# Optimization experiments

Hardware: AMD Instinct MI355X
Metric: run time of the kernel (lower is better)

The kernel has to match this reference:

```python
import jax, jax.numpy as jnp
import numpy as np

# Kobayashi dendrite-growth parameters (init_params values from the repo)
TAU = 3e-4
EPSILONB = 0.01
KAPPA = 1.8
DELTA = 0.02
ANISO = 6.0
ALPHA = 0.9
GAMMA = 10.0
TEQ = 1.0
THETA0 = 0.2
PIX = 4.0 * np.arctan(1.0)  # pi
DX = 0.03
DY = 0.03
DT = 1e-4

B, H, W = 4, 2048, 2048


def lap(u, dx, dy):
    # 5-point Laplacian, periodic boundaries. x = last axis, y = second-to-last.
    return ((jnp.roll(u, -1, -1) + jnp.roll(u, 1, -1) - 2.0 * u) / (dx * dx)
            + (jnp.roll(u, -1, -2) + jnp.roll(u, 1, -2) - 2.0 * u) / (dy * dy))


def grad(u, axis_name, d):
    ax = -1 if axis_name == 'x' else -2
    return (jnp.roll(u, -1, ax) - jnp.roll(u, 1, ax)) / (2.0 * d)


def setup_inputs() -> dict:
    key = jax.random.key(0)
    k1, k2 = jax.random.split(key)
    phi = jax.random.uniform(k1, (B, H, W), dtype=jnp.float32)
    tempr = jax.random.uniform(k2, (B, H, W), dtype=jnp.float32)
    return {"phi": phi, "tempr": tempr}


def reference(phi, tempr):
    lap_phi = lap(phi, DX, DY)
    lap_tempr = lap(tempr, DX, DY)
    phidx = grad(phi, 'x', DX)
    phidy = grad(phi, 'y', DY)
    theta = jnp.arctan2(phidy, phidx)
    epsilon = EPSILONB * (1.0 + DELTA * jnp.cos(ANISO * (theta - THETA0)))
    epsilon_deriv = -EPSILONB * ANISO * DELTA * jnp.sin(ANISO * (theta - THETA0))
    prod_mat1 = epsilon * epsilon_deriv * phidx
    prod_mat2 = -epsilon * epsilon_deriv * phidy
    term1 = grad(prod_mat1, 'y', DY)
    term2 = grad(prod_mat2, 'x', DX)
    m = ALPHA / PIX * jnp.arctan(GAMMA * (TEQ - tempr))
    dphi_dt = DT / TAU * (term1 + term2 + epsilon ** 2 * lap_phi
                          + phi * (1.0 - phi) * (phi - 0.5 + m))
    phi_new = phi + dphi_dt
    tempr_new = tempr + DT * lap_tempr + KAPPA * dphi_dt
    return (phi_new, tempr_new)
```

## Files before the change

### kernel.cpp

```cpp
#include <hip/hip_runtime.h>
#include <hip/hip_fp16.h>
#include <math.h>


#define Bz 4
#define Hd 2048
#define Wd 2048
#define TX 64
#define TY 32
#define PW 68
#define PH 36
#define QW 66
#define QH 34

#define INVD2   1111.11111111111f
#define K1      277.777777777778f
#define DT_TAU  0.333333333333333f
#define DTc     1e-4f
#define KAPPAc  1.8f
#define EPSB    0.01f
#define DELTAc  0.02f
#define ANISOc  6.0f
#define A_PI    0.2864788975654116f
#define GAMMAc  10.0f
#define TEQc    1.0f
#define C6T0    0.3623577544766736f
#define S6T0    0.9320390859672263f
#define PI_2    1.5707963267948966f
#define SC      65536.0f
#define ISC     (1.0f/65536.0f)

__device__ __forceinline__ void prodc(float dx, float dy,
                                      float& p1s, float& p2s, float& e2s)
{
    float dx2 = dx * dx;
    float r2  = fmaf(dy, dy, dx2);
    float cn  = fmaf(-dy, dy, dx2);
    float irr = __builtin_amdgcn_rcpf(fmaxf(r2, 1e-20f));
    float c2  = cn * irr;
    float s2  = 2.0f * dx * dy * irr;
    float c22 = c2 * c2;
    float s22 = s2 * s2;
    float c6  = c2 * fmaf(4.0f, c22, -3.0f);
    float s6  = s2 * fmaf(-4.0f, s22, 3.0f);
    float cosA = fmaf(c6, C6T0, s6 * S6T0);
    float sinA = fmaf(s6, C6T0, -c6 * S6T0);
    float eps  = fmaf(EPSB * DELTAc, cosA, EPSB);
    float eesc = eps * (-EPSB * ANISOc * DELTAc * SC) * sinA;
    p1s = eesc * dx;
    p2s = -eesc * dy;
    e2s = eps * eps * SC;
}

__device__ __forceinline__ float atan_fast(float g) {
    float r  = __builtin_amdgcn_rcpf(g);
    float a  = fminf(g, r);
    float a2 = a * a;
    float p  = a * fmaf(a2, fmaf(a2, 0.079331f, -0.288679f), 0.995354f);
    return (g <= 1.0f) ? p : PI_2 - p;
}

__global__ __launch_bounds__(256, 8) void dendrite_step(
    const float* __restrict__ phi, const float* __restrict__ tempr,
    float* __restrict__ out_phi, float* __restrict__ out_tempr)
{
    __shared__ __half2 sphi2[PH * PW / 2];
    __shared__ __half2 spk[QH * QW];
    __shared__ __half2 se2_2[QH * QW / 2];

    const int tid = threadIdx.x;
    const int x0 = blockIdx.x * TX;
    const int y0 = blockIdx.y * TY;
    const int base = blockIdx.z * (Hd * Wd);

    for (int i = tid; i < PH * PW / 2; i += 256) {
        int r = i / (PW / 2);
        int c2 = i - r * (PW / 2);
        int gy = (y0 + r - 2) & (Hd - 1);
        int gx = (x0 + 2 * c2 - 2) & (Wd - 1);
        float2 v = *(const float2*)(phi + base + gy * Wd + gx);
        sphi2[i] = __floats2half2_rn(v.x, v.y);
    }
    __syncthreads();

    const __half* sph = (const __half*)sphi2;
    for (int i = tid; i < QH * (QW / 2); i += 256) {
        int r = i / (QW / 2);
        int c2 = i - r * (QW / 2);
        int cQ = 2 * c2;
        int rowc = (r + 1) * (PW / 2) + c2;
        __half2 A  = sphi2[rowc];
        __half2 Bv = sphi2[rowc + 1];
        __half2 U0 = sphi2[rowc - PW / 2];
        __half2 U1 = sphi2[rowc - PW / 2 + 1];
        __half2 D0 = sphi2[rowc + PW / 2];
        __half2 D1 = sphi2[rowc + PW / 2 + 1];

        float f0 = __low2float(A),  f1 = __high2float(A);
        float f2 = __low2float(Bv), f3 = __high2float(Bv);

        float p1a, p2a, e2a, p1b, p2b, e2b;
        prodc(f2 - f0, __high2float(D0) - __high2float(U0), p1a, p2a, e2a);
        prodc(f3 - f1, __low2float(D1)  - __low2float(U1),  p1b, p2b, e2b);

        int q = r * QW + cQ;
        spk[q]     = __floats2half2_rn(p1a, p2a);
        spk[q + 1] = __floats2half2_rn(p1b, p2b);
        se2_2[r * (QW / 2) + c2] = __floats2half2_rn(e2a, e2b);
    }
    __syncthreads();

    const __half* se2h = (const __half*)se2_2;
    const int tx = tid & 63;
    const int tg = tid >> 6;
    const int ys = tg * 8;
    const int col = tx + 2;
    const int gx = x0 + tx;
    const int gxm = (gx - 1) & (Wd - 1);
    const int gxp = (gx + 1) & (Wd - 1);

    float pm = __half2float(sph[(ys + 1) * PW + col]);
    float pc_ = __half2float(sph[(ys + 2) * PW + col]);
    float s1m = __low2float(spk[ys * QW + tx + 1]);
    float s1c = __low2float(spk[(ys + 1) * QW + tx + 1]);

    float tm = tempr[base + ((y0 + ys - 1) & (Hd - 1)) * Wd + gx];
    int rb0 = base + (y0 + ys) * Wd;
    float tcl = tempr[rb0 + gxm];
    float tcc = tempr[rb0 + gx];
    float tcr = tempr[rb0 + gxp];
    int rb1 = base + ((y0 + ys + 1) & (Hd - 1)) * Wd;
    float tnl = tempr[rb1 + gxm];
    float tnc = tempr[rb1 + gx];
    float tnr = tempr[rb1 + gxp];

    for (int k = 0; k < 8; ++k) {
        int y = ys + k;
        int qrow = y + 1;
        int prow = y + 2;

        float t2l = 0.0f, t2c = 0.0f, t2r = 0.0f;
        if (k < 7) {
            int rb2 = base + ((y0 + y + 2) & (Hd - 1)) * Wd;
            t2l = tempr[rb2 + gxm];
            t2c = tempr[rb2 + gx];
            t2r = tempr[rb2 + gxp];
        }

        float pp  = __half2float(sph[(prow + 1) * PW + col]);
        float pl  = __half2float(sph[prow * PW + col - 1]);
        float prr = __half2float(sph[prow * PW + col + 1]);
        float lap_phi = (pl + prr + pm + pp - 4.0f * pc_) * INVD2;

        float s1p  = __low2float(spk[(qrow + 1) * QW + tx + 1]);
        float sp2l = __high2float(spk[qrow * QW + tx]);
        float sp2r = __high2float(spk[qrow * QW + tx + 2]);
        float term12 = (s1p - s1m + sp2r - sp2l) * (K1 * ISC);
        float e2 = __half2float(se2h[qrow * QW + tx + 1]) * ISC;

        float lap_t = (tcl + tcr + tm + tnc - 4.0f * tcc) * INVD2;

        float mm = A_PI * atan_fast(GAMMAc * (TEQc - tcc));
        float dphi = DT_TAU * (term12 + e2 * lap_phi
                               + pc_ * (1.0f - pc_) * (pc_ - 0.5f + mm));

        int gidx = base + (y0 + y) * Wd + gx;
        out_phi[gidx] = pc_ + dphi;
        out_tempr[gidx] = fmaf(KAPPAc, dphi, fmaf(DTc, lap_t, tcc));

        pm = pc_; pc_ = pp;
        s1m = s1c; s1c = s1p;
        tm = tcc;
        tcl = tnl; tcc = tnc; tcr = tnr;
        tnl = t2l; tnc = t2c; tnr = t2r;
    }
}

extern "C" void kernel_launch(void* const* d_in, const int* in_sizes, int n_in,
                              void* d_out, int out_size, void* d_ws, size_t ws_size,
                              hipStream_t stream) {
    const float* phi = (const float*)d_in[0];
    const float* tempr = (const float*)d_in[1];
    float* out_phi = (float*)d_out;
    float* out_tempr = out_phi + (size_t)Bz * Hd * Wd;

    dim3 grid(Wd / TX, Hd / TY, Bz);
    dendrite_step<<<grid, 256, 0, stream>>>(phi, tempr, out_phi, out_tempr);
}
```

Measured before the change: 240.6 us.

## Process two columns per thread with vectorized half2/float2 LDS and global access

Each thread now computes two adjacent x-columns across 4 rows instead of one column across 8 rows. Shared-memory padding is widened to 4 columns so halo reads align to half2. Reads and writes of phi/products, tempr and outputs become 2-wide vector accesses, and neighbour values are shared between the pair. This targets LDS instruction count and global transaction count, at the cost of more registers per thread and shorter row-streaming reuse.

```diff
diff --git a/kernel.cpp b/kernel.cpp
--- a/kernel.cpp
+++ b/kernel.cpp
@@ -8,9 +8,10 @@
 #define Wd 2048
 #define TX 64
 #define TY 32
-#define PW 68
+#define PW 72
 #define PH 36
-#define QW 66
+#define PW2 (PW/2)
+#define QW 68
 #define QH 34
 
 #define INVD2   1111.11111111111f
@@ -60,119 +61,166 @@
     return (g <= 1.0f) ? p : PI_2 - p;
 }
 
+__device__ __forceinline__ void ldq2(const __half2* p,
+                                     float& f1a, float& f2a,
+                                     float& f1b, float& f2b)
+{
+    uint2 v = *reinterpret_cast<const uint2*>(p);
+    __half2 a = *reinterpret_cast<__half2*>(&v.x);
+    __half2 b = *reinterpret_cast<__half2*>(&v.y);
+    f1a = __low2float(a); f2a = __high2float(a);
+    f1b = __low2float(b); f2b = __high2float(b);
+}
+
 __global__ __launch_bounds__(256, 8) void dendrite_step(
     const float* __restrict__ phi, const float* __restrict__ tempr,
     float* __restrict__ out_phi, float* __restrict__ out_tempr)
 {
-    __shared__ __half2 sphi2[PH * PW / 2];
+    __shared__ __half2 sphi2[PH * PW2];
     __shared__ __half2 spk[QH * QW];
-    __shared__ __half2 se2_2[QH * QW / 2];
+    __shared__ __half  se2[QH * QW];
 
     const int tid = threadIdx.x;
     const int x0 = blockIdx.x * TX;
     const int y0 = blockIdx.y * TY;
     const int base = blockIdx.z * (Hd * Wd);
 
-    for (int i = tid; i < PH * PW / 2; i += 256) {
-        int r = i / (PW / 2);
-        int c2 = i - r * (PW / 2);
+    for (int i = tid; i < PH * PW2; i += 256) {
+        int r = i / PW2;
+        int c2 = i - r * PW2;
         int gy = (y0 + r - 2) & (Hd - 1);
-        int gx = (x0 + 2 * c2 - 2) & (Wd - 1);
+        int gx = (x0 + 2 * c2 - 4) & (Wd - 1);
         float2 v = *(const float2*)(phi + base + gy * Wd + gx);
         sphi2[i] = __floats2half2_rn(v.x, v.y);
     }
     __syncthreads();
 
-    const __half* sph = (const __half*)sphi2;
     for (int i = tid; i < QH * (QW / 2); i += 256) {
         int r = i / (QW / 2);
-        int c2 = i - r * (QW / 2);
-        int cQ = 2 * c2;
-        int rowc = (r + 1) * (PW / 2) + c2;
-        __half2 A  = sphi2[rowc];
-        __half2 Bv = sphi2[rowc + 1];
-        __half2 U0 = sphi2[rowc - PW / 2];
-        __half2 U1 = sphi2[rowc - PW / 2 + 1];
-        __half2 D0 = sphi2[rowc + PW / 2];
-        __half2 D1 = sphi2[rowc + PW / 2 + 1];
-
-        float f0 = __low2float(A),  f1 = __high2float(A);
-        float f2 = __low2float(Bv), f3 = __high2float(Bv);
+        int j = i - r * (QW / 2);
+        int rowc = (r + 1) * PW2 + j;
+        __half2 P0 = sphi2[rowc];
+        __half2 P1 = sphi2[rowc + 1];
+        __half2 P2 = sphi2[rowc + 2];
+        __half2 U  = sphi2[rowc - PW2 + 1];
+        __half2 D  = sphi2[rowc + PW2 + 1];
+
+        float dx0 = __high2float(P1) - __high2float(P0);
+        float dx1 = __low2float(P2)  - __low2float(P1);
+        float dy0 = __low2float(D)   - __low2float(U);
+        float dy1 = __high2float(D)  - __high2float(U);
 
         float p1a, p2a, e2a, p1b, p2b, e2b;
-        prodc(f2 - f0, __high2float(D0) - __high2float(U0), p1a, p2a, e2a);
-        prodc(f3 - f1, __low2float(D1)  - __low2float(U1),  p1b, p2b, e2b);
-
-        int q = r * QW + cQ;
+        prodc(dx0, dy0, p1a, p2a, e2a);
+        prodc(dx1, dy1, p1b, p2b, e2b);
+
+        int q = r * QW + 2 * j;
         spk[q]     = __floats2half2_rn(p1a, p2a);
         spk[q + 1] = __floats2half2_rn(p1b, p2b);
-        se2_2[r * (QW / 2) + c2] = __floats2half2_rn(e2a, e2b);
+        *reinterpret_cast<__half2*>(se2 + q) = __floats2half2_rn(e2a, e2b);
     }
     __syncthreads();
 
-    const __half* se2h = (const __half*)se2_2;
-    const int tx = tid & 63;
-    const int tg = tid >> 6;
-    const int ys = tg * 8;
-    const int col = tx + 2;
-    const int gx = x0 + tx;
-    const int gxm = (gx - 1) & (Wd - 1);
-    const int gxp = (gx + 1) & (Wd - 1);
-
-    float pm = __half2float(sph[(ys + 1) * PW + col]);
-    float pc_ = __half2float(sph[(ys + 2) * PW + col]);
-    float s1m = __low2float(spk[ys * QW + tx + 1]);
-    float s1c = __low2float(spk[(ys + 1) * QW + tx + 1]);
-
-    float tm = tempr[base + ((y0 + ys - 1) & (Hd - 1)) * Wd + gx];
+    const int tx2 = tid & 31;
+    const int tg  = tid >> 5;
+    const int ys  = tg * 4;
+    const int c0  = tx2 * 2;
+    const int qc0 = c0 + 2;
+    const int pctr = (c0 + 4) >> 1;
+    const int gx0 = x0 + c0;
+    const int gxm = (gx0 - 1) & (Wd - 1);
+    const int gxp = (gx0 + 2) & (Wd - 1);
+
+    float pm0, pm1, pc0, pc1;
+    {
+        __half2 a = sphi2[(ys + 1) * PW2 + pctr];
+        __half2 b = sphi2[(ys + 2) * PW2 + pctr];
+        pm0 = __low2float(a); pm1 = __high2float(a);
+        pc0 = __low2float(b); pc1 = __high2float(b);
+    }
+
+    float s1m0 = __low2float(spk[ys * QW + qc0]);
+    float s1m1 = __low2float(spk[ys * QW + qc0 + 1]);
+    float s1c0, p2c0, s1c1, p2c1;
+    ldq2(spk + (ys + 1) * QW + qc0, s1c0, p2c0, s1c1, p2c1);
+
+    float tm0, tm1;
+    {
+        float2 t = *(const float2*)(tempr + base + ((y0 + ys - 1) & (Hd - 1)) * Wd + gx0);
+        tm0 = t.x; tm1 = t.y;
+    }
     int rb0 = base + (y0 + ys) * Wd;
     float tcl = tempr[rb0 + gxm];
-    float tcc = tempr[rb0 + gx];
+    float2 tc0v = *(const float2*)(tempr + rb0 + gx0);
+    float tcc0 = tc0v.x, tcc1 = tc0v.y;
     float tcr = tempr[rb0 + gxp];
     int rb1 = base + ((y0 + ys + 1) & (Hd - 1)) * Wd;
     float tnl = tempr[rb1 + gxm];
-    float tnc = tempr[rb1 + gx];
+    float2 tn0v = *(const float2*)(tempr + rb1 + gx0);
+    float tnc0 = tn0v.x, tnc1 = tn0v.y;
     float tnr = tempr[rb1 + gxp];
 
-    for (int k = 0; k < 8; ++k) {
+    for (int k = 0; k < 4; ++k) {
         int y = ys + k;
         int qrow = y + 1;
         int prow = y + 2;
 
-        float t2l = 0.0f, t2c = 0.0f, t2r = 0.0f;
-        if (k < 7) {
+        float t2l = 0.0f, t2c0 = 0.0f, t2c1 = 0.0f, t2r = 0.0f;
+        if (k < 3) {
             int rb2 = base + ((y0 + y + 2) & (Hd - 1)) * Wd;
             t2l = tempr[rb2 + gxm];
-            t2c = tempr[rb2 + gx];
+            float2 t2 = *(const float2*)(tempr + rb2 + gx0);
+            t2c0 = t2.x; t2c1 = t2.y;
             t2r = tempr[rb2 + gxp];
         }
 
-        float pp  = __half2float(sph[(prow + 1) * PW + col]);
-        float pl  = __half2float(sph[prow * PW + col - 1]);
-        float prr = __half2float(sph[prow * PW + col + 1]);
-        float lap_phi = (pl + prr + pm + pp - 4.0f * pc_) * INVD2;
-
-        float s1p  = __low2float(spk[(qrow + 1) * QW + tx + 1]);
-        float sp2l = __high2float(spk[qrow * QW + tx]);
-        float sp2r = __high2float(spk[qrow * QW + tx + 2]);
-        float term12 = (s1p - s1m + sp2r - sp2l) * (K1 * ISC);
-        float e2 = __half2float(se2h[qrow * QW + tx + 1]) * ISC;
-
-        float lap_t = (tcl + tcr + tm + tnc - 4.0f * tcc) * INVD2;
-
-        float mm = A_PI * atan_fast(GAMMAc * (TEQc - tcc));
-        float dphi = DT_TAU * (term12 + e2 * lap_phi
-                               + pc_ * (1.0f - pc_) * (pc_ - 0.5f + mm));
-
-        int gidx = base + (y0 + y) * Wd + gx;
-        out_phi[gidx] = pc_ + dphi;
-        out_tempr[gidx] = fmaf(KAPPAc, dphi, fmaf(DTc, lap_t, tcc));
-
-        pm = pc_; pc_ = pp;
-        s1m = s1c; s1c = s1p;
-        tm = tcc;
-        tcl = tnl; tcc = tnc; tcr = tnr;
-        tnl = t2l; tnc = t2c; tnr = t2r;
+        __half2 hpp = sphi2[(prow + 1) * PW2 + pctr];
+        __half2 hL  = sphi2[prow * PW2 + pctr - 1];
+        __half2 hR  = sphi2[prow * PW2 + pctr + 1];
+        float pp0 = __low2float(hpp), pp1 = __high2float(hpp);
+        float pl  = __high2float(hL);
+        float pr  = __low2float(hR);
+
+        float lap0 = (pl  + pc1 + pm0 + pp0 - 4.0f * pc0) * INVD2;
+        float lap1 = (pc0 + pr  + pm1 + pp1 - 4.0f * pc1) * INVD2;
+
+        float s1p0, p2n0, s1p1, p2n1;
+        ldq2(spk + (qrow + 1) * QW + qc0, s1p0, p2n0, s1p1, p2n1);
+
+        float sp2l = __high2float(spk[qrow * QW + qc0 - 1]);
+        float sp2r = __high2float(spk[qrow * QW + qc0 + 2]);
+
+        __half2 he2 = *reinterpret_cast<const __half2*>(se2 + qrow * QW + qc0);
+        float e20 = __low2float(he2) * ISC;
+        float e21 = __high2float(he2) * ISC;
+
+        float t120 = (s1p0 - s1m0 + p2c1 - sp2l) * (K1 * ISC);
+        float t121 = (s1p1 - s1m1 + sp2r - p2c0) * (K1 * ISC);
+
+        float lt0 = (tcl  + tcc1 + tm0 + tnc0 - 4.0f * tcc0) * INVD2;
+        float lt1 = (tcc0 + tcr  + tm1 + tnc1 - 4.0f * tcc1) * INVD2;
+
+        float mm0 = A_PI * atan_fast(GAMMAc * (TEQc - tcc0));
+        float mm1 = A_PI * atan_fast(GAMMAc * (TEQc - tcc1));
+
+        float dphi0 = DT_TAU * (t120 + e20 * lap0
+                                + pc0 * (1.0f - pc0) * (pc0 - 0.5f + mm0));
+        float dphi1 = DT_TAU * (t121 + e21 * lap1
+                                + pc1 * (1.0f - pc1) * (pc1 - 0.5f + mm1));
+
+        int gidx = base + (y0 + y) * Wd + gx0;
+        *(float2*)(out_phi + gidx) =
+            make_float2(pc0 + dphi0, pc1 + dphi1);
+        *(float2*)(out_tempr + gidx) =
+            make_float2(fmaf(KAPPAc, dphi0, fmaf(DTc, lt0, tcc0)),
+                        fmaf(KAPPAc, dphi1, fmaf(DTc, lt1, tcc1)));
+
+        pm0 = pc0; pm1 = pc1; pc0 = pp0; pc1 = pp1;
+        s1m0 = s1c0; s1m1 = s1c1; s1c0 = s1p0; s1c1 = s1p1;
+        p2c0 = p2n0; p2c1 = p2n1;
+        tm0 = tcc0; tm1 = tcc1;
+        tcl = tnl; tcc0 = tnc0; tcc1 = tnc1; tcr = tnr;
+        tnl = t2l; tnc0 = t2c0; tnc1 = t2c1; tnr = t2r;
     }
 }
 
```

Measured after the change: 241.5 us. Within noise of the previous version (+0.4%).

## Replace shared-memory fp16 tiling with per-wave register streaming and lane shuffles

Applied to the files above, without the earlier changes.

The kernel drops the shared-memory tile of half-precision phi, product terms and epsilon squared. Each wavefront now streams down a 32-row column strip in registers, using cross-lane shuffles for horizontal neighbours and edge lanes loading halo values directly. This removes both block-wide barriers and the fp16 rounding, and cuts redundant halo work. In exchange it adds divergent edge-lane branches and recomputes the p2 term for halo columns, and occupancy now depends on register pressure instead of LDS use.

```diff
diff --git a/kernel.cpp b/kernel.cpp
--- a/kernel.cpp
+++ b/kernel.cpp
@@ -1,20 +1,15 @@
 #include <hip/hip_runtime.h>
-#include <hip/hip_fp16.h>
 #include <math.h>
 
 
 #define Bz 4
 #define Hd 2048
 #define Wd 2048
-#define TX 64
-#define TY 32
-#define PW 68
-#define PH 36
-#define QW 66
-#define QH 34
+#define SH 32
+#define WPB 4
 
 #define INVD2   1111.11111111111f
-#define K1      277.777777777778f
+#define K1c     277.777777777778f
 #define DT_TAU  0.333333333333333f
 #define DTc     1e-4f
 #define KAPPAc  1.8f
@@ -27,11 +22,9 @@
 #define C6T0    0.3623577544766736f
 #define S6T0    0.9320390859672263f
 #define PI_2    1.5707963267948966f
-#define SC      65536.0f
-#define ISC     (1.0f/65536.0f)
 
 __device__ __forceinline__ void prodc(float dx, float dy,
-                                      float& p1s, float& p2s, float& e2s)
+                                      float& p1, float& p2, float& e2)
 {
     float dx2 = dx * dx;
     float r2  = fmaf(dy, dy, dx2);
@@ -39,17 +32,15 @@
     float irr = __builtin_amdgcn_rcpf(fmaxf(r2, 1e-20f));
     float c2  = cn * irr;
     float s2  = 2.0f * dx * dy * irr;
-    float c22 = c2 * c2;
-    float s22 = s2 * s2;
-    float c6  = c2 * fmaf(4.0f, c22, -3.0f);
-    float s6  = s2 * fmaf(-4.0f, s22, 3.0f);
+    float c6  = c2 * fmaf(4.0f, c2 * c2, -3.0f);
+    float s6  = s2 * fmaf(-4.0f, s2 * s2, 3.0f);
     float cosA = fmaf(c6, C6T0, s6 * S6T0);
     float sinA = fmaf(s6, C6T0, -c6 * S6T0);
     float eps  = fmaf(EPSB * DELTAc, cosA, EPSB);
-    float eesc = eps * (-EPSB * ANISOc * DELTAc * SC) * sinA;
-    p1s = eesc * dx;
-    p2s = -eesc * dy;
-    e2s = eps * eps * SC;
+    float ee   = eps * (-EPSB * ANISOc * DELTAc) * sinA;
+    p1 = ee * dx;
+    p2 = -ee * dy;
+    e2 = eps * eps;
 }
 
 __device__ __forceinline__ float atan_fast(float g) {
@@ -60,119 +51,131 @@
     return (g <= 1.0f) ? p : PI_2 - p;
 }
 
-__global__ __launch_bounds__(256, 8) void dendrite_step(
+__global__ __launch_bounds__(256) void dendrite_step(
     const float* __restrict__ phi, const float* __restrict__ tempr,
     float* __restrict__ out_phi, float* __restrict__ out_tempr)
 {
-    __shared__ __half2 sphi2[PH * PW / 2];
-    __shared__ __half2 spk[QH * QW];
-    __shared__ __half2 se2_2[QH * QW / 2];
+    const int tid  = threadIdx.x;
+    const int lane = tid & 63;
+    const int wv   = tid >> 6;
+    const int x0   = blockIdx.x * 64;
+    const int y0   = blockIdx.y * (WPB * SH) + wv * SH;
+    const int base = blockIdx.z * (Hd * Wd);
+    const int gx   = x0 + lane;
 
-    const int tid = threadIdx.x;
-    const int x0 = blockIdx.x * TX;
-    const int y0 = blockIdx.y * TY;
-    const int base = blockIdx.z * (Hd * Wd);
+    const bool eL = (lane == 0);
+    const bool eR = (lane == 63);
+    const bool eE = eL || eR;
+    const int hxc = eL ? ((x0 - 2) & (Wd - 1)) : ((x0 + 64) & (Wd - 1));
+    const int thx = eL ? ((x0 - 1) & (Wd - 1)) : ((x0 + 64) & (Wd - 1));
 
-    for (int i = tid; i < PH * PW / 2; i += 256) {
-        int r = i / (PW / 2);
-        int c2 = i - r * (PW / 2);
-        int gy = (y0 + r - 2) & (Hd - 1);
-        int gx = (x0 + 2 * c2 - 2) & (Wd - 1);
-        float2 v = *(const float2*)(phi + base + gy * Wd + gx);
-        sphi2[i] = __floats2half2_rn(v.x, v.y);
+    auto prow = [&](const float* a, int r) {
+        return a + base + ((y0 + r) & (Hd - 1)) * Wd;
+    };
+
+    float pc_m2 = prow(phi, -2)[gx];
+    float pc_m1 = prow(phi, -1)[gx];
+    float pc_0  = prow(phi,  0)[gx];
+    float pc_p1 = prow(phi,  1)[gx];
+    float pc_p2 = prow(phi,  2)[gx];
+    float tm = prow(tempr, -1)[gx];
+    float tc = prow(tempr,  0)[gx];
+    float tn = prow(tempr,  1)[gx];
+
+    float2 Hmm = make_float2(0.f, 0.f), Hm = Hmm, Hc = Hmm, Hp = Hmm;
+    float tH_c = 0.0f;
+    if (eE) {
+        Hmm = *(const float2*)(prow(phi, -1) + hxc);
+        Hm  = *(const float2*)(prow(phi,  0) + hxc);
+        Hc  = *(const float2*)(prow(phi,  1) + hxc);
+        Hp  = *(const float2*)(prow(phi,  2) + hxc);
+        tH_c = prow(tempr, 0)[thx];
     }
-    __syncthreads();
 
-    const __half* sph = (const __half*)sphi2;
-    for (int i = tid; i < QH * (QW / 2); i += 256) {
-        int r = i / (QW / 2);
-        int c2 = i - r * (QW / 2);
-        int cQ = 2 * c2;
-        int rowc = (r + 1) * (PW / 2) + c2;
-        __half2 A  = sphi2[rowc];
-        __half2 Bv = sphi2[rowc + 1];
-        __half2 U0 = sphi2[rowc - PW / 2];
-        __half2 U1 = sphi2[rowc - PW / 2 + 1];
-        __half2 D0 = sphi2[rowc + PW / 2];
-        __half2 D1 = sphi2[rowc + PW / 2 + 1];
+    float plm = __shfl_up(pc_m1, 1), prm = __shfl_down(pc_m1, 1);
+    float plc = __shfl_up(pc_0, 1),  prc = __shfl_down(pc_0, 1);
+    if (eL) { plm = Hmm.y; plc = Hm.y; }
+    if (eR) { prm = Hmm.x; prc = Hm.x; }
+    float tlc = __shfl_up(tc, 1), trc = __shfl_down(tc, 1);
+    if (eL) tlc = tH_c;
+    if (eR) trc = tH_c;
 
-        float f0 = __low2float(A),  f1 = __high2float(A);
-        float f2 = __low2float(Bv), f3 = __high2float(Bv);
+    float p1m, p1c, p2c, e2c, du0, du1;
+    prodc(prm - plm, pc_0 - pc_m2, p1m, du0, du1);
+    prodc(prc - plc, pc_p1 - pc_m1, p1c, p2c, e2c);
 
-        float p1a, p2a, e2a, p1b, p2b, e2b;
-        prodc(f2 - f0, __high2float(D0) - __high2float(U0), p1a, p2a, e2a);
-        prodc(f3 - f1, __low2float(D1)  - __low2float(U1),  p1b, p2b, e2b);
+    float p2h_c = 0.0f;
+    if (eE) {
+        float dxh = eL ? (pc_0 - Hm.x) : (Hm.y - pc_0);
+        float mp  = eL ? Hc.y  : Hc.x;
+        float mmv = eL ? Hmm.y : Hmm.x;
+        float a, c_;
+        prodc(dxh, mp - mmv, a, p2h_c, c_);
+        (void)a; (void)c_;
+    }
 
-        int q = r * QW + cQ;
-        spk[q]     = __floats2half2_rn(p1a, p2a);
-        spk[q + 1] = __floats2half2_rn(p1b, p2b);
-        se2_2[r * (QW / 2) + c2] = __floats2half2_rn(e2a, e2b);
-    }
-    __syncthreads();
+    const int omask = Hd * Wd - 1;
+    int oP  = ((y0 + 3) & (Hd - 1)) * Wd;
+    int oT  = ((y0 + 2) & (Hd - 1)) * Wd;
+    int oTH = ((y0 + 1) & (Hd - 1)) * Wd;
+    int gout = base + y0 * Wd + gx;
 
-    const __half* se2h = (const __half*)se2_2;
-    const int tx = tid & 63;
-    const int tg = tid >> 6;
-    const int ys = tg * 8;
-    const int col = tx + 2;
-    const int gx = x0 + tx;
-    const int gxm = (gx - 1) & (Wd - 1);
-    const int gxp = (gx + 1) & (Wd - 1);
-
-    float pm = __half2float(sph[(ys + 1) * PW + col]);
-    float pc_ = __half2float(sph[(ys + 2) * PW + col]);
-    float s1m = __low2float(spk[ys * QW + tx + 1]);
-    float s1c = __low2float(spk[(ys + 1) * QW + tx + 1]);
-
-    float tm = tempr[base + ((y0 + ys - 1) & (Hd - 1)) * Wd + gx];
-    int rb0 = base + (y0 + ys) * Wd;
-    float tcl = tempr[rb0 + gxm];
-    float tcc = tempr[rb0 + gx];
-    float tcr = tempr[rb0 + gxp];
-    int rb1 = base + ((y0 + ys + 1) & (Hd - 1)) * Wd;
-    float tnl = tempr[rb1 + gxm];
-    float tnc = tempr[rb1 + gx];
-    float tnr = tempr[rb1 + gxp];
-
-    for (int k = 0; k < 8; ++k) {
-        int y = ys + k;
-        int qrow = y + 1;
-        int prow = y + 2;
-
-        float t2l = 0.0f, t2c = 0.0f, t2r = 0.0f;
-        if (k < 7) {
-            int rb2 = base + ((y0 + y + 2) & (Hd - 1)) * Wd;
-            t2l = tempr[rb2 + gxm];
-            t2c = tempr[rb2 + gx];
-            t2r = tempr[rb2 + gxp];
+    #pragma unroll 4
+    for (int k = 0; k < SH; ++k) {
+        float ph_new = phi[base + oP + gx];
+        float t_new  = tempr[base + oT + gx];
+        float2 H_new = make_float2(0.f, 0.f);
+        float tH_n = 0.0f;
+        if (eE) {
+            H_new = *(const float2*)(phi + base + oP + hxc);
+            tH_n  = tempr[base + oTH + thx];
         }
 
-        float pp  = __half2float(sph[(prow + 1) * PW + col]);
-        float pl  = __half2float(sph[prow * PW + col - 1]);
-        float prr = __half2float(sph[prow * PW + col + 1]);
-        float lap_phi = (pl + prr + pm + pp - 4.0f * pc_) * INVD2;
+        float pl1 = __shfl_up(pc_p1, 1), pr1 = __shfl_down(pc_p1, 1);
+        if (eL) pl1 = Hc.y;
+        if (eR) pr1 = Hc.x;
+        float p1p, p2n, e2n;
+        prodc(pr1 - pl1, pc_p2 - pc_0, p1p, p2n, e2n);
 
-        float s1p  = __low2float(spk[(qrow + 1) * QW + tx + 1]);
-        float sp2l = __high2float(spk[qrow * QW + tx]);
-        float sp2r = __high2float(spk[qrow * QW + tx + 2]);
-        float term12 = (s1p - s1m + sp2r - sp2l) * (K1 * ISC);
-        float e2 = __half2float(se2h[qrow * QW + tx + 1]) * ISC;
+        float p2h_n = 0.0f;
+        if (eE) {
+            float dxh = eL ? (pc_p1 - Hc.x) : (Hc.y - pc_p1);
+            float mp  = eL ? Hp.y : Hp.x;
+            float mmv = eL ? Hm.y : Hm.x;
+            float a, c_;
+            prodc(dxh, mp - mmv, a, p2h_n, c_);
+            (void)a; (void)c_;
+        }
 
-        float lap_t = (tcl + tcr + tm + tnc - 4.0f * tcc) * INVD2;
+        float tl_n = __shfl_up(tn, 1), tr_n = __shfl_down(tn, 1);
+        if (eL) tl_n = tH_n;
+        if (eR) tr_n = tH_n;
 
-        float mm = A_PI * atan_fast(GAMMAc * (TEQc - tcc));
-        float dphi = DT_TAU * (term12 + e2 * lap_phi
-                               + pc_ * (1.0f - pc_) * (pc_ - 0.5f + mm));
+        float p2l = __shfl_up(p2c, 1), p2r = __shfl_down(p2c, 1);
+        if (eL) p2l = p2h_c;
+        if (eR) p2r = p2h_c;
 
-        int gidx = base + (y0 + y) * Wd + gx;
-        out_phi[gidx] = pc_ + dphi;
-        out_tempr[gidx] = fmaf(KAPPAc, dphi, fmaf(DTc, lap_t, tcc));
+        float t12  = (p1p - p1m + p2r - p2l) * K1c;
+        float lapp = (plc + prc + pc_m1 + pc_p1 - 4.0f * pc_0) * INVD2;
+        float lapt = (tlc + trc + tm + tn - 4.0f * tc) * INVD2;
+        float mval = A_PI * atan_fast(GAMMAc * (TEQc - tc));
+        float dphi = DT_TAU * (t12 + e2c * lapp
+                       + pc_0 * (1.0f - pc_0) * (pc_0 - 0.5f + mval));
+        out_phi[gout]   = pc_0 + dphi;
+        out_tempr[gout] = fmaf(KAPPAc, dphi, fmaf(DTc, lapt, tc));
 
-        pm = pc_; pc_ = pp;
-        s1m = s1c; s1c = s1p;
-        tm = tcc;
-        tcl = tnl; tcc = tnc; tcr = tnr;
-        tnl = t2l; tnc = t2c; tnr = t2r;
+        pc_m1 = pc_0; pc_0 = pc_p1; pc_p1 = pc_p2; pc_p2 = ph_new;
+        plc = pl1; prc = pr1;
+        p1m = p1c; p1c = p1p;
+        p2c = p2n; e2c = e2n; p2h_c = p2h_n;
+        tm = tc; tc = tn; tn = t_new;
+        tlc = tl_n; trc = tr_n;
+        Hm = Hc; Hc = Hp; Hp = H_new;
+
+        oP  = (oP  + Wd) & omask;
+        oT  = (oT  + Wd) & omask;
+        oTH = (oTH + Wd) & omask;
+        gout += Wd;
     }
 }
 
@@ -184,6 +187,6 @@
     float* out_phi = (float*)d_out;
     float* out_tempr = out_phi + (size_t)Bz * Hd * Wd;
 
-    dim3 grid(Wd / TX, Hd / TY, Bz);
+    dim3 grid(Wd / 64, Hd / (WPB * SH), Bz);
     dendrite_step<<<grid, 256, 0, stream>>>(phi, tempr, out_phi, out_tempr);
 }
```

Result: slower. 250.6 us (+4.1%).
